# Optimization experiments

Measured on AMD Instinct MI355X. Metric: run time of the kernel, lower is better.

Reference implementation:

```python
import jax, jax.numpy as jnp
import numpy as np

NU = 200000   # num user nodes
NI = 200000   # num item nodes
E = 500000    # edges per relation
D = 128       # in_feats
H = 128       # h_feats
NEG_SLOPE = 0.01  # F.leaky_relu default


def _sage(x_src, x_dst, src, dst, n_dst, W_self, W_neigh, b):
    # DGL SAGEConv('mean'): fc_self(x_dst) + fc_neigh(mean of in-neighbors) + bias
    msg = x_src[src]                                   # [E, d] gather
    agg = jax.ops.segment_sum(msg, dst, num_segments=n_dst)   # [n_dst, d]
    deg = jax.ops.segment_sum(jnp.ones((src.shape[0],), x_src.dtype), dst,
                              num_segments=n_dst)      # [n_dst]
    mean = agg / jnp.maximum(deg, 1.0)[:, None]        # zero in-degree -> 0
    return x_dst @ W_self + mean @ W_neigh + b


def setup_inputs() -> dict:
    key = jax.random.key(0)
    ks = jax.random.split(key, 20)
    s = 1.0 / np.sqrt(D)
    inp = {
        'x_user': jax.random.normal(ks[0], (NU, D), jnp.float32),
        'x_item': jax.random.normal(ks[1], (NI, D), jnp.float32),
        'w1_self_uc': jax.random.normal(ks[2], (D, H), jnp.float32) * s,
        'w1_neigh_uc': jax.random.normal(ks[3], (D, H), jnp.float32) * s,
        'b1_uc': jnp.zeros((H,), jnp.float32),
        'w1_self_iu': jax.random.normal(ks[4], (D, H), jnp.float32) * s,
        'w1_neigh_iu': jax.random.normal(ks[5], (D, H), jnp.float32) * s,
        'b1_iu': jnp.zeros((H,), jnp.float32),
        'w2_self_uc': jax.random.normal(ks[6], (H, H), jnp.float32) * s,
        'w2_neigh_uc': jax.random.normal(ks[7], (H, H), jnp.float32) * s,
        'b2_uc': jnp.zeros((H,), jnp.float32),
        'w2_self_iu': jax.random.normal(ks[8], (H, H), jnp.float32) * s,
        'w2_neigh_iu': jax.random.normal(ks[9], (H, H), jnp.float32) * s,
        'b2_iu': jnp.zeros((H,), jnp.float32),
        'src_uc': jax.random.randint(ks[10], (E,), 0, NU, jnp.int32),
        'dst_uc': jax.random.randint(ks[11], (E,), 0, NI, jnp.int32),
        'src_iu': jax.random.randint(ks[12], (E,), 0, NI, jnp.int32),
        'dst_iu': jax.random.randint(ks[13], (E,), 0, NU, jnp.int32),
    }
    return inp


def reference(x_user, x_item,
              w1_self_uc, w1_neigh_uc, b1_uc, w1_self_iu, w1_neigh_iu, b1_iu,
              w2_self_uc, w2_neigh_uc, b2_uc, w2_self_iu, w2_neigh_iu, b2_iu,
              src_uc, dst_uc, src_iu, dst_iu):
    # layer 1: relation 'clicks' user->item, relation 'clicked_by' item->user
    h1_item = _sage(x_user, x_item, src_uc, dst_uc, NI, w1_self_uc, w1_neigh_uc, b1_uc)
    h1_user = _sage(x_item, x_user, src_iu, dst_iu, NU, w1_self_iu, w1_neigh_iu, b1_iu)
    h1_item = jax.nn.leaky_relu(h1_item, NEG_SLOPE)
    h1_user = jax.nn.leaky_relu(h1_user, NEG_SLOPE)
    # layer 2
    h2_item = _sage(h1_user, h1_item, src_uc, dst_uc, NI, w2_self_uc, w2_neigh_uc, b2_uc)
    h2_user = _sage(h1_item, h1_user, src_iu, dst_iu, NU, w2_self_iu, w2_neigh_iu, b2_iu)
    # stack [user, item] (same shape) for a single output tensor
    return jnp.stack([h2_user, h2_item], axis=0)  # [2, 200000, 128]
```

## Files before the change

kernel.cpp:

```cpp
#include <hip/hip_runtime.h>
#include <hip/hip_bf16.h>

#define D_ 128
#define H_ 128

typedef __attribute__((ext_vector_type(8))) short s8b;
typedef __attribute__((ext_vector_type(4))) float f4;

union U4 { uint u[4]; s8b v; uint4 q; };

__global__ void deg2_kernel(const int* __restrict__ dstA, const int* __restrict__ dstB,
                            int* __restrict__ degA, int* __restrict__ degB, int E) {
    int e = blockIdx.x * blockDim.x + threadIdx.x;
    const int* dst = blockIdx.y ? dstB : dstA;
    int* deg = blockIdx.y ? degB : degA;
    if (e < E) atomicAdd(&deg[dst[e]], 1);
}

__global__ __launch_bounds__(256)
void scan1m(const int* __restrict__ degA, const int* __restrict__ degB,
            int* __restrict__ rpA, int* __restrict__ rpB,
            int* __restrict__ partA, int* __restrict__ partB, int N) {
    const int* deg = blockIdx.y ? degB : degA;
    int* rp = blockIdx.y ? rpB : rpA;
    int* partials = blockIdx.y ? partB : partA;
    int tid = threadIdx.x;
    int i = blockIdx.x * 256 + tid;
    int v = (i < N) ? deg[i] : 0;
    int lane = tid & 63, wid = tid >> 6;
    int x = v;
#pragma unroll
    for (int off = 1; off < 64; off <<= 1) {
        int y = __shfl_up(x, off, 64);
        if (lane >= off) x += y;
    }
    __shared__ int wsum[5];
    if (lane == 63) wsum[wid] = x;
    __syncthreads();
    if (tid == 0) {
        int a = wsum[0], b = wsum[1], c = wsum[2], d = wsum[3];
        wsum[0] = 0; wsum[1] = a; wsum[2] = a + b; wsum[3] = a + b + c;
        wsum[4] = a + b + c + d;
    }
    __syncthreads();
    if (i < N) rp[i] = wsum[wid] + x - v;
    if (tid == 0) partials[blockIdx.x] = wsum[4];
}

__global__ __launch_bounds__(1024)
void scan2m(int* __restrict__ partA, int* __restrict__ partB, int B) {
    int* partials = blockIdx.x ? partB : partA;
    __shared__ int buf[1024];
    int t = threadIdx.x;
    int v = (t < B) ? partials[t] : 0;
    buf[t] = v;
    __syncthreads();
    for (int off = 1; off < 1024; off <<= 1) {
        int add = (t >= off) ? buf[t - off] : 0;
        __syncthreads();
        buf[t] += add;
        __syncthreads();
    }
    if (t < B) partials[t] = buf[t] - v;
}

__global__ __launch_bounds__(256)
void scan3m(int* __restrict__ rpA, int* __restrict__ rpB,
            const int* __restrict__ partA, const int* __restrict__ partB, int N, int E) {
    int* rp = blockIdx.y ? rpB : rpA;
    const int* partials = blockIdx.y ? partB : partA;
    int i = blockIdx.x * 256 + threadIdx.x;
    if (i < N) rp[i] += partials[blockIdx.x];
    if (i == 0) rp[N] = E;
}

__global__ void fill2_csr(const int* __restrict__ srcA, const int* __restrict__ dstA,
                          const int* __restrict__ rpA, int* __restrict__ curA,
                          int* __restrict__ colA, int* __restrict__ colpA,
                          const int* __restrict__ srcB, const int* __restrict__ dstB,
                          const int* __restrict__ rpB, int* __restrict__ curB,
                          int* __restrict__ colB, int* __restrict__ colpB, int E) {
    int e = blockIdx.x * blockDim.x + threadIdx.x;
    if (e >= E) return;
    const int* src = blockIdx.y ? srcB : srcA;
    const int* dst = blockIdx.y ? dstB : dstA;
    const int* rp  = blockIdx.y ? rpB : rpA;
    int* cursor = blockIdx.y ? curB : curA;
    int* col    = blockIdx.y ? colB : colA;
    int* colp   = blockIdx.y ? colpB : colpA;
    int d = dst[e];
    int s = src[e];
    int idx = atomicAdd(&cursor[d], 1);
    col[rp[d] + idx] = s;
    if (idx < 4) colp[d * 4 + idx] = s;
}

__device__ __forceinline__ void fma4(float4& a, const float4& u, float w) {
    a.x = fmaf(u.x, w, a.x); a.y = fmaf(u.y, w, a.y);
    a.z = fmaf(u.z, w, a.z); a.w = fmaf(u.w, w, a.w);
}

__device__ __forceinline__ void gather_node(const float* __restrict__ x,
                                            const int* __restrict__ rp,
                                            const int* __restrict__ col,
                                            const int* __restrict__ colp,
                                            float* __restrict__ out,
                                            int node, int li) {
    int beg = rp[node];
    int end = rp[node + 1];
    int dg = end - beg;
    int4 c4 = *(const int4*)(colp + (size_t)node * 4);
    int s0 = dg > 0 ? c4.x : 0;
    int s1 = dg > 1 ? c4.y : 0;
    int s2 = dg > 2 ? c4.z : 0;
    int s3 = dg > 3 ? c4.w : 0;
    const float4* p0 = (const float4*)(x + (size_t)s0 * 128 + li * 8);
    const float4* p1 = (const float4*)(x + (size_t)s1 * 128 + li * 8);
    const float4* p2 = (const float4*)(x + (size_t)s2 * 128 + li * 8);
    const float4* p3 = (const float4*)(x + (size_t)s3 * 128 + li * 8);
    float4 u00 = p0[0], u01 = p0[1];
    float4 u10 = p1[0], u11 = p1[1];
    float4 u20 = p2[0], u21 = p2[1];
    float4 u30 = p3[0], u31 = p3[1];
    float w0 = dg > 0 ? 1.f : 0.f;
    float w1 = dg > 1 ? 1.f : 0.f;
    float w2 = dg > 2 ? 1.f : 0.f;
    float w3 = dg > 3 ? 1.f : 0.f;
    float4 a0 = make_float4(0.f, 0.f, 0.f, 0.f);
    float4 a1 = make_float4(0.f, 0.f, 0.f, 0.f);
    fma4(a0, u00, w0); fma4(a1, u01, w0);
    fma4(a0, u10, w1); fma4(a1, u11, w1);
    fma4(a0, u20, w2); fma4(a1, u21, w2);
    fma4(a0, u30, w3); fma4(a1, u31, w3);
    for (int e = beg + 4; e < end; ++e) {
        int s = col[e];
        const float4* p = (const float4*)(x + (size_t)s * 128 + li * 8);
        float4 v0 = p[0], v1 = p[1];
        a0.x += v0.x; a0.y += v0.y; a0.z += v0.z; a0.w += v0.w;
        a1.x += v1.x; a1.y += v1.y; a1.z += v1.z; a1.w += v1.w;
    }
    float inv = 1.0f / (float)(dg > 0 ? dg : 1);
    float4 o0 = make_float4(a0.x * inv, a0.y * inv, a0.z * inv, a0.w * inv);
    float4 o1 = make_float4(a1.x * inv, a1.y * inv, a1.z * inv, a1.w * inv);
    float4* q = (float4*)(out + (size_t)node * 128 + li * 8);
    q[0] = o0;
    q[1] = o1;
}

__global__ __launch_bounds__(256)
void gather2(const float* __restrict__ xA, const int* __restrict__ rpA,
             const int* __restrict__ colA, const int* __restrict__ colpA,
             float* __restrict__ outA, int NA,
             const float* __restrict__ xB, const int* __restrict__ rpB,
             const int* __restrict__ colB, const int* __restrict__ colpB,
             float* __restrict__ outB, int NB, int blocksA) {
    bool isA = (int)blockIdx.x < blocksA;
    int bid = isA ? blockIdx.x : blockIdx.x - blocksA;
    long long gid = (long long)bid * 256 + threadIdx.x;
    int node = (int)(gid >> 4);
    int li = (int)(gid & 15);
    if (isA) {
        if (node < NA) gather_node(xA, rpA, colA, colpA, outA, node, li);
    } else {
        if (node < NB) gather_node(xB, rpB, colB, colpB, outB, node, li);
    }
}

__global__ __launch_bounds__(256)
void prep_weights(const float* __restrict__ s0, const float* __restrict__ n0,
                  const float* __restrict__ s1, const float* __restrict__ n1,
                  const float* __restrict__ s2, const float* __restrict__ n2,
                  const float* __restrict__ s3, const float* __restrict__ n3,
                  ushort* __restrict__ WTH, ushort* __restrict__ WTL) {
    int g = blockIdx.y;
    int t = blockIdx.x * 256 + threadIdx.x;
    int c = t & 127;
    int oct = t >> 7;
    const float* self  = g == 0 ? s0 : g == 1 ? s1 : g == 2 ? s2 : s3;
    const float* neigh = g == 0 ? n0 : g == 1 ? n1 : g == 2 ? n2 : n3;
    uint hd[4], ld_[4];
#pragma unroll
    for (int p = 0; p < 4; ++p) {
        uint hpair = 0, lpair = 0;
#pragma unroll
        for (int q = 0; q < 2; ++q) {
            int kv = oct * 8 + p * 2 + q;
            const float* Wsrc = kv < 128 ? self : neigh;
            float f = Wsrc[(size_t)(kv & 127) * 128 + c];
            uint u = __float_as_uint(f);
            uint h = u >> 16;
            float r = f - __uint_as_float(u & 0xffff0000u);
            uint v = __float_as_uint(r);
            uint l = (v + 0x7fffu + ((v >> 16) & 1u)) >> 16;
            hpair |= h << (16 * q);
            lpair |= l << (16 * q);
        }
        hd[p] = hpair; ld_[p] = lpair;
    }
    size_t base = ((size_t)g * 128 + c) * 256 + oct * 8;
    *(uint4*)(WTH + base) = make_uint4(hd[0], hd[1], hd[2], hd[3]);
    *(uint4*)(WTL + base) = make_uint4(ld_[0], ld_[1], ld_[2], ld_[3]);
}

__device__ __forceinline__ void gemm_body(const float* __restrict__ A1,
                                          const float* __restrict__ A2,
                                          const ushort* __restrict__ WTh,
                                          const ushort* __restrict__ WTl,
                                          const float* __restrict__ bias,
                                          float* __restrict__ out,
                                          int N, int lrelu, int bid,
                                          s8b* ldsAh, s8b* ldsAl, s8b* ldsWh, s8b* ldsWl) {
    const int t = threadIdx.x;
    const int row0 = bid * 128;
    const int lane = t & 63, w = t >> 6;
    const int mrow0 = (w & 1) * 64, ncol0 = (w >> 1) * 64;
    const int fr = lane & 15, hi = lane >> 4;

    f4 acc[4][4];
    float bv[4];
#pragma unroll
    for (int n = 0; n < 4; ++n) bv[n] = bias[ncol0 + n * 16 + fr];
#pragma unroll
    for (int m = 0; m < 4; ++m)
#pragma unroll
        for (int n = 0; n < 4; ++n) acc[m][n] = (f4){bv[n], bv[n], bv[n], bv[n]};

    const int sr = t >> 1, half = t & 1;
    const int grow = row0 + sr;
    const int swz = (sr >> 1) & 3;

    int aslot[4], wslot[4];
#pragma unroll
    for (int m = 0; m < 4; ++m) {
        int r = mrow0 + m * 16 + fr;
        aslot[m] = r * 4 + (hi ^ ((r >> 1) & 3));
    }
#pragma unroll
    for (int n = 0; n < 4; ++n) {
        int c = ncol0 + n * 16 + fr;
        wslot[n] = c * 4 + (hi ^ ((c >> 1) & 3));
    }

    for (int ks = 0; ks < 8; ++ks) {
        const float* __restrict__ As = (ks < 4) ? A1 : A2;
        const int k0 = (ks & 3) * 32 + half * 16;
        float e[16];
        if (grow < N) {
            const float4* p = (const float4*)(As + (size_t)grow * 128 + k0);
            float4 q0 = p[0], q1 = p[1], q2 = p[2], q3 = p[3];
            e[0] = q0.x; e[1] = q0.y; e[2] = q0.z; e[3] = q0.w;
            e[4] = q1.x; e[5] = q1.y; e[6] = q1.z; e[7] = q1.w;
            e[8] = q2.x; e[9] = q2.y; e[10] = q2.z; e[11] = q2.w;
            e[12] = q3.x; e[13] = q3.y; e[14] = q3.z; e[15] = q3.w;
        } else {
#pragma unroll
            for (int i = 0; i < 16; ++i) e[i] = 0.f;
        }
        uint hd[8], ld_[8];
#pragma unroll
        for (int p = 0; p < 8; ++p) {
            uint u0 = __float_as_uint(e[2 * p]);
            uint u1 = __float_as_uint(e[2 * p + 1]);
            hd[p] = (u0 >> 16) | (u1 & 0xffff0000u);
            float r0 = e[2 * p] - __uint_as_float(u0 & 0xffff0000u);
            float r1 = e[2 * p + 1] - __uint_as_float(u1 & 0xffff0000u);
            uint v0 = __float_as_uint(r0), v1 = __float_as_uint(r1);
            uint l0 = (v0 + 0x7fffu + ((v0 >> 16) & 1u)) >> 16;
            uint l1 = (v1 + 0x7fffu + ((v1 >> 16) & 1u)) >> 16;
            ld_[p] = l0 | (l1 << 16);
        }
        {
            U4 a0; a0.u[0] = hd[0]; a0.u[1] = hd[1]; a0.u[2] = hd[2]; a0.u[3] = hd[3];
            U4 a1; a1.u[0] = hd[4]; a1.u[1] = hd[5]; a1.u[2] = hd[6]; a1.u[3] = hd[7];
            U4 b0; b0.u[0] = ld_[0]; b0.u[1] = ld_[1]; b0.u[2] = ld_[2]; b0.u[3] = ld_[3];
            U4 b1; b1.u[0] = ld_[4]; b1.u[1] = ld_[5]; b1.u[2] = ld_[6]; b1.u[3] = ld_[7];
            int h0 = half * 2, h1 = half * 2 + 1;
            ldsAh[sr * 4 + (h0 ^ swz)] = a0.v;
            ldsAh[sr * 4 + (h1 ^ swz)] = a1.v;
            ldsAl[sr * 4 + (h0 ^ swz)] = b0.v;
            ldsAl[sr * 4 + (h1 ^ swz)] = b1.v;
        }
        {
            size_t wbase = (size_t)sr * 256 + ks * 32 + half * 16;
            U4 wh0, wh1, wl0, wl1;
            wh0.q = *(const uint4*)(WTh + wbase);
            wh1.q = *(const uint4*)(WTh + wbase + 8);
            wl0.q = *(const uint4*)(WTl + wbase);
            wl1.q = *(const uint4*)(WTl + wbase + 8);
            int h0 = half * 2, h1 = half * 2 + 1;
            ldsWh[sr * 4 + (h0 ^ swz)] = wh0.v;
            ldsWh[sr * 4 + (h1 ^ swz)] = wh1.v;
            ldsWl[sr * 4 + (h0 ^ swz)] = wl0.v;
            ldsWl[sr * 4 + (h1 ^ swz)] = wl1.v;
        }
        __syncthreads();

        s8b ah[4], al[4];
#pragma unroll
        for (int m = 0; m < 4; ++m) { ah[m] = ldsAh[aslot[m]]; al[m] = ldsAl[aslot[m]]; }
#pragma unroll
        for (int n = 0; n < 4; ++n) {
            s8b wh = ldsWh[wslot[n]];
            s8b wl = ldsWl[wslot[n]];
#pragma unroll
            for (int m = 0; m < 4; ++m) {
                acc[m][n] = __builtin_amdgcn_mfma_f32_16x16x32_bf16(ah[m], wh, acc[m][n], 0, 0, 0);
                acc[m][n] = __builtin_amdgcn_mfma_f32_16x16x32_bf16(al[m], wh, acc[m][n], 0, 0, 0);
                acc[m][n] = __builtin_amdgcn_mfma_f32_16x16x32_bf16(ah[m], wl, acc[m][n], 0, 0, 0);
            }
        }
        __syncthreads();
    }

#pragma unroll
    for (int m = 0; m < 4; ++m) {
#pragma unroll
        for (int r = 0; r < 4; ++r) {
            int row = row0 + mrow0 + m * 16 + hi * 4 + r;
            if (row >= N) continue;
#pragma unroll
            for (int n = 0; n < 4; ++n) {
                float v = acc[m][n][r];
                if (lrelu) v = v > 0.f ? v : 0.01f * v;
                out[(size_t)row * 128 + ncol0 + n * 16 + fr] = v;
            }
        }
    }
}

__global__ __launch_bounds__(256)
void gemm2(const float* __restrict__ A1a, const float* __restrict__ A2a,
           const ushort* __restrict__ WTha, const ushort* __restrict__ WTla,
           const float* __restrict__ ba, float* __restrict__ outa, int Na,
           const float* __restrict__ A1b, const float* __restrict__ A2b,
           const ushort* __restrict__ WThb, const ushort* __restrict__ WTlb,
           const float* __restrict__ bb, float* __restrict__ outb, int Nb,
           int blocksA, int lrelu) {
    __shared__ s8b ldsAh[512];
    __shared__ s8b ldsAl[512];
    __shared__ s8b ldsWh[512];
    __shared__ s8b ldsWl[512];
    bool isA = (int)blockIdx.x < blocksA;
    int bid = isA ? blockIdx.x : blockIdx.x - blocksA;
    if (isA)
        gemm_body(A1a, A2a, WTha, WTla, ba, outa, Na, lrelu, bid, ldsAh, ldsAl, ldsWh, ldsWl);
    else
        gemm_body(A1b, A2b, WThb, WTlb, bb, outb, Nb, lrelu, bid, ldsAh, ldsAl, ldsWh, ldsWl);
}

extern "C" void kernel_launch(void* const* d_in, const int* in_sizes, int n_in,
                              void* d_out, int out_size, void* d_ws, size_t ws_size,
                              hipStream_t stream) {
    const float* x_user     = (const float*)d_in[0];
    const float* x_item     = (const float*)d_in[1];
    const float* w1_self_uc = (const float*)d_in[2];
    const float* w1_neigh_uc= (const float*)d_in[3];
    const float* b1_uc      = (const float*)d_in[4];
    const float* w1_self_iu = (const float*)d_in[5];
    const float* w1_neigh_iu= (const float*)d_in[6];
    const float* b1_iu      = (const float*)d_in[7];
    const float* w2_self_uc = (const float*)d_in[8];
    const float* w2_neigh_uc= (const float*)d_in[9];
    const float* b2_uc      = (const float*)d_in[10];
    const float* w2_self_iu = (const float*)d_in[11];
    const float* w2_neigh_iu= (const float*)d_in[12];
    const float* b2_iu      = (const float*)d_in[13];
    const int* src_uc = (const int*)d_in[14];
    const int* dst_uc = (const int*)d_in[15];
    const int* src_iu = (const int*)d_in[16];
    const int* dst_iu = (const int*)d_in[17];

    const int NU = in_sizes[0] / D_;
    const int NI = in_sizes[1] / D_;
    const int E  = in_sizes[14];

    float* out_user = (float*)d_out;
    float* out_item = (float*)d_out + (size_t)NU * H_;

    char* ws = (char*)d_ws;
    const size_t FEAT_BYTES = (size_t)200000 * 128 * sizeof(float);
    float* agg_i   = (float*)ws;  ws += FEAT_BYTES;
    float* agg_u   = (float*)ws;  ws += FEAT_BYTES;
    ushort* WTH    = (ushort*)ws; ws += (size_t)4 * 128 * 256 * sizeof(ushort);
    ushort* WTL    = (ushort*)ws; ws += (size_t)4 * 128 * 256 * sizeof(ushort);
    int* colp_uc   = (int*)ws;    ws += (size_t)200000 * 4 * sizeof(int);
    int* colp_iu   = (int*)ws;    ws += (size_t)200000 * 4 * sizeof(int);
    int* rp_uc     = (int*)ws;    ws += (size_t)(NI + 1) * sizeof(int);
    int* rp_iu     = (int*)ws;    ws += (size_t)(NU + 1) * sizeof(int);
    int* col_uc    = (int*)ws;    ws += (size_t)E * sizeof(int);
    int* col_iu    = (int*)ws;    ws += (size_t)E * sizeof(int);
    int* deg_uc    = (int*)ws;    ws += (size_t)200000 * sizeof(int);
    int* deg_iu    = (int*)ws;    ws += (size_t)200000 * sizeof(int);
    int* cur_uc    = (int*)ws;    ws += (size_t)200000 * sizeof(int);
    int* cur_iu    = (int*)ws;    ws += (size_t)200000 * sizeof(int);
    int* partA     = (int*)ws;    ws += (size_t)1024 * sizeof(int);
    int* partB     = (int*)ws;    ws += (size_t)1024 * sizeof(int);

    const int TPB = 256;
    const int eBlocks  = (E + TPB - 1) / TPB;
    const int sBlocks  = (200000 + 255) / 256;
    const int gBlocksI = (int)(((long long)NI * 16 + TPB - 1) / TPB);
    const int gBlocksU = (int)(((long long)NU * 16 + TPB - 1) / TPB);
    const int mBlocksI = (NI + 127) / 128;
    const int mBlocksU = (NU + 127) / 128;
    const size_t WSTRIDE = (size_t)128 * 256;

    hipMemsetAsync(deg_uc, 0, (size_t)4 * 200000 * sizeof(int), stream);

    prep_weights<<<dim3(16, 4), 256, 0, stream>>>(
        w1_self_uc, w1_neigh_uc, w1_self_iu, w1_neigh_iu,
        w2_self_uc, w2_neigh_uc, w2_self_iu, w2_neigh_iu, WTH, WTL);

    deg2_kernel<<<dim3(eBlocks, 2), TPB, 0, stream>>>(dst_uc, dst_iu, deg_uc, deg_iu, E);
    scan1m<<<dim3(sBlocks, 2), 256, 0, stream>>>(deg_uc, deg_iu, rp_uc, rp_iu, partA, partB, 200000);
    scan2m<<<2, 1024, 0, stream>>>(partA, partB, sBlocks);
    scan3m<<<dim3(sBlocks, 2), 256, 0, stream>>>(rp_uc, rp_iu, partA, partB, 200000, E);
    fill2_csr<<<dim3(eBlocks, 2), TPB, 0, stream>>>(src_uc, dst_uc, rp_uc, cur_uc, col_uc, colp_uc,
                                                    src_iu, dst_iu, rp_iu, cur_iu, col_iu, colp_iu, E);

    gather2<<<gBlocksI + gBlocksU, TPB, 0, stream>>>(
        x_user, rp_uc, col_uc, colp_uc, agg_i, NI,
        x_item, rp_iu, col_iu, colp_iu, agg_u, NU, gBlocksI);
    gemm2<<<mBlocksI + mBlocksU, TPB, 0, stream>>>(
        x_item, agg_i, WTH + 0 * WSTRIDE, WTL + 0 * WSTRIDE, b1_uc, out_item, NI,
        x_user, agg_u, WTH + 1 * WSTRIDE, WTL + 1 * WSTRIDE, b1_iu, out_user, NU,
        mBlocksI, 1);

    gather2<<<gBlocksI + gBlocksU, TPB, 0, stream>>>(
        out_user, rp_uc, col_uc, colp_uc, agg_i, NI,
        out_item, rp_iu, col_iu, colp_iu, agg_u, NU, gBlocksI);
    gemm2<<<mBlocksI + mBlocksU, TPB, 0, stream>>>(
        out_item, agg_i, WTH + 2 * WSTRIDE, WTL + 2 * WSTRIDE, b2_uc, out_item, NI,
        out_user, agg_u, WTH + 3 * WSTRIDE, WTL + 3 * WSTRIDE, b2_iu, out_user, NU,
        mBlocksI, 0);
}
```

Baseline: 645.2 us.

## Store intermediates as pre-split bf16 hi/lo and double-buffer GEMM via direct LDS loads

Result: slower. 770.4 us (+19.4%).

```diff
diff --git a/kernel.cpp b/kernel.cpp
--- a/kernel.cpp
+++ b/kernel.cpp
@@ -2,12 +2,28 @@
 #include <hip/hip_bf16.h>
 
 #define D_ 128
-#define H_ 128
 
 typedef __attribute__((ext_vector_type(8))) short s8b;
 typedef __attribute__((ext_vector_type(4))) float f4;
 
 union U4 { uint u[4]; s8b v; uint4 q; };
+
+__device__ __forceinline__ void gl16(const void* g, void* lds) {
+    __builtin_amdgcn_global_load_lds(
+        (const __attribute__((address_space(1))) void*)g,
+        (__attribute__((address_space(3))) void*)lds, 16, 0, 0);
+}
+
+__device__ __forceinline__ void split2(float f0, float f1, uint& hp, uint& lp) {
+    uint u0 = __float_as_uint(f0), u1 = __float_as_uint(f1);
+    hp = (u0 >> 16) | (u1 & 0xffff0000u);
+    float r0 = f0 - __uint_as_float(u0 & 0xffff0000u);
+    float r1 = f1 - __uint_as_float(u1 & 0xffff0000u);
+    uint v0 = __float_as_uint(r0), v1 = __float_as_uint(r1);
+    uint l0 = (v0 + 0x7fffu + ((v0 >> 16) & 1u)) >> 16;
+    uint l1 = (v1 + 0x7fffu + ((v1 >> 16) & 1u)) >> 16;
+    lp = l0 | (l1 << 16);
+}
 
 __global__ void deg2_kernel(const int* __restrict__ dstA, const int* __restrict__ dstB,
                             int* __restrict__ degA, int* __restrict__ degB, int E) {
@@ -95,75 +111,97 @@
     if (idx < 4) colp[d * 4 + idx] = s;
 }
 
-__device__ __forceinline__ void fma4(float4& a, const float4& u, float w) {
-    a.x = fmaf(u.x, w, a.x); a.y = fmaf(u.y, w, a.y);
-    a.z = fmaf(u.z, w, a.z); a.w = fmaf(u.w, w, a.w);
-}
-
-__device__ __forceinline__ void gather_node(const float* __restrict__ x,
-                                            const int* __restrict__ rp,
-                                            const int* __restrict__ col,
-                                            const int* __restrict__ colp,
-                                            float* __restrict__ out,
-                                            int node, int li) {
-    int beg = rp[node];
-    int end = rp[node + 1];
+__device__ __forceinline__ void acc8hl(float* a, uint4 h4, uint4 l4, float wgt) {
+    const ushort* hu = (const ushort*)&h4;
+    const ushort* lu = (const ushort*)&l4;
+#pragma unroll
+    for (int j = 0; j < 8; ++j) {
+        float v = __uint_as_float((uint)hu[j] << 16) + __uint_as_float((uint)lu[j] << 16);
+        a[j] = fmaf(v, wgt, a[j]);
+    }
+}
+__device__ __forceinline__ void acc8f(float* a, float4 u0, float4 u1, float wgt) {
+    a[0] = fmaf(u0.x, wgt, a[0]); a[1] = fmaf(u0.y, wgt, a[1]);
+    a[2] = fmaf(u0.z, wgt, a[2]); a[3] = fmaf(u0.w, wgt, a[3]);
+    a[4] = fmaf(u1.x, wgt, a[4]); a[5] = fmaf(u1.y, wgt, a[5]);
+    a[6] = fmaf(u1.z, wgt, a[6]); a[7] = fmaf(u1.w, wgt, a[7]);
+}
+
+template<int INHL>
+__device__ __forceinline__ void gather_node(const char* x, const int* rp,
+        const int* col, const int* colp, ushort* out, int node, int li) {
+    int beg = rp[node], end = rp[node + 1];
     int dg = end - beg;
     int4 c4 = *(const int4*)(colp + (size_t)node * 4);
     int s0 = dg > 0 ? c4.x : 0;
     int s1 = dg > 1 ? c4.y : 0;
     int s2 = dg > 2 ? c4.z : 0;
     int s3 = dg > 3 ? c4.w : 0;
-    const float4* p0 = (const float4*)(x + (size_t)s0 * 128 + li * 8);
-    const float4* p1 = (const float4*)(x + (size_t)s1 * 128 + li * 8);
-    const float4* p2 = (const float4*)(x + (size_t)s2 * 128 + li * 8);
-    const float4* p3 = (const float4*)(x + (size_t)s3 * 128 + li * 8);
-    float4 u00 = p0[0], u01 = p0[1];
-    float4 u10 = p1[0], u11 = p1[1];
-    float4 u20 = p2[0], u21 = p2[1];
-    float4 u30 = p3[0], u31 = p3[1];
     float w0 = dg > 0 ? 1.f : 0.f;
     float w1 = dg > 1 ? 1.f : 0.f;
     float w2 = dg > 2 ? 1.f : 0.f;
     float w3 = dg > 3 ? 1.f : 0.f;
-    float4 a0 = make_float4(0.f, 0.f, 0.f, 0.f);
-    float4 a1 = make_float4(0.f, 0.f, 0.f, 0.f);
-    fma4(a0, u00, w0); fma4(a1, u01, w0);
-    fma4(a0, u10, w1); fma4(a1, u11, w1);
-    fma4(a0, u20, w2); fma4(a1, u21, w2);
-    fma4(a0, u30, w3); fma4(a1, u31, w3);
+    float a[8];
+#pragma unroll
+    for (int j = 0; j < 8; ++j) a[j] = 0.f;
+
+    if (INHL) {
+        const char* p0 = x + (size_t)s0 * 512 + li * 16;
+        const char* p1 = x + (size_t)s1 * 512 + li * 16;
+        const char* p2 = x + (size_t)s2 * 512 + li * 16;
+        const char* p3 = x + (size_t)s3 * 512 + li * 16;
+        uint4 H0 = *(const uint4*)p0, L0 = *(const uint4*)(p0 + 256);
+        uint4 H1 = *(const uint4*)p1, L1 = *(const uint4*)(p1 + 256);
+        uint4 H2 = *(const uint4*)p2, L2 = *(const uint4*)(p2 + 256);
+        uint4 H3 = *(const uint4*)p3, L3 = *(const uint4*)(p3 + 256);
+        acc8hl(a, H0, L0, w0); acc8hl(a, H1, L1, w1);
+        acc8hl(a, H2, L2, w2); acc8hl(a, H3, L3, w3);
+    } else {
+        const char* p0 = x + (size_t)s0 * 512 + li * 32;
+        const char* p1 = x + (size_t)s1 * 512 + li * 32;
+        const char* p2 = x + (size_t)s2 * 512 + li * 32;
+        const char* p3 = x + (size_t)s3 * 512 + li * 32;
+        float4 A0 = *(const float4*)p0, B0 = *(const float4*)(p0 + 16);
+        float4 A1 = *(const float4*)p1, B1 = *(const float4*)(p1 + 16);
+        float4 A2 = *(const float4*)p2, B2 = *(const float4*)(p2 + 16);
+        float4 A3 = *(const float4*)p3, B3 = *(const float4*)(p3 + 16);
+        acc8f(a, A0, B0, w0); acc8f(a, A1, B1, w1);
+        acc8f(a, A2, B2, w2); acc8f(a, A3, B3, w3);
+    }
     for (int e = beg + 4; e < end; ++e) {
         int s = col[e];
-        const float4* p = (const float4*)(x + (size_t)s * 128 + li * 8);
-        float4 v0 = p[0], v1 = p[1];
-        a0.x += v0.x; a0.y += v0.y; a0.z += v0.z; a0.w += v0.w;
-        a1.x += v1.x; a1.y += v1.y; a1.z += v1.z; a1.w += v1.w;
-    }
-    float inv = 1.0f / (float)(dg > 0 ? dg : 1);
-    float4 o0 = make_float4(a0.x * inv, a0.y * inv, a0.z * inv, a0.w * inv);
-    float4 o1 = make_float4(a1.x * inv, a1.y * inv, a1.z * inv, a1.w * inv);
-    float4* q = (float4*)(out + (size_t)node * 128 + li * 8);
-    q[0] = o0;
-    q[1] = o1;
-}
-
+        if (INHL) {
+            const char* p = x + (size_t)s * 512 + li * 16;
+            acc8hl(a, *(const uint4*)p, *(const uint4*)(p + 256), 1.f);
+        } else {
+            const char* p = x + (size_t)s * 512 + li * 32;
+            acc8f(a, *(const float4*)p, *(const float4*)(p + 16), 1.f);
+        }
+    }
+    float inv = 1.f / (float)(dg > 0 ? dg : 1);
+    uint h0, h1, h2, h3, l0, l1, l2, l3;
+    split2(a[0] * inv, a[1] * inv, h0, l0);
+    split2(a[2] * inv, a[3] * inv, h1, l1);
+    split2(a[4] * inv, a[5] * inv, h2, l2);
+    split2(a[6] * inv, a[7] * inv, h3, l3);
+    char* ob = (char*)out + (size_t)node * 512;
+    *(uint4*)(ob + li * 16) = make_uint4(h0, h1, h2, h3);
+    *(uint4*)(ob + 256 + li * 16) = make_uint4(l0, l1, l2, l3);
+}
+
+template<int INHL>
 __global__ __launch_bounds__(256)
-void gather2(const float* __restrict__ xA, const int* __restrict__ rpA,
-             const int* __restrict__ colA, const int* __restrict__ colpA,
-             float* __restrict__ outA, int NA,
-             const float* __restrict__ xB, const int* __restrict__ rpB,
-             const int* __restrict__ colB, const int* __restrict__ colpB,
-             float* __restrict__ outB, int NB, int blocksA) {
+void gather2k(const void* xA, const int* rpA, const int* colA, const int* colpA,
+              ushort* outA, int NA,
+              const void* xB, const int* rpB, const int* colB, const int* colpB,
+              ushort* outB, int NB, int blocksA) {
     bool isA = (int)blockIdx.x < blocksA;
     int bid = isA ? blockIdx.x : blockIdx.x - blocksA;
     long long gid = (long long)bid * 256 + threadIdx.x;
     int node = (int)(gid >> 4);
     int li = (int)(gid & 15);
-    if (isA) {
-        if (node < NA) gather_node(xA, rpA, colA, colpA, outA, node, li);
-    } else {
-        if (node < NB) gather_node(xB, rpB, colB, colpB, outB, node, li);
-    }
+    if (isA) { if (node < NA) gather_node<INHL>((const char*)xA, rpA, colA, colpA, outA, node, li); }
+    else     { if (node < NB) gather_node<INHL>((const char*)xB, rpB, colB, colpB, outB, node, li); }
 }
 
 __global__ __launch_bounds__(256)
@@ -202,150 +240,172 @@
     *(uint4*)(WTL + base) = make_uint4(ld_[0], ld_[1], ld_[2], ld_[3]);
 }
 
-__device__ __forceinline__ void gemm_body(const float* __restrict__ A1,
-                                          const float* __restrict__ A2,
-                                          const ushort* __restrict__ WTh,
-                                          const ushort* __restrict__ WTl,
-                                          const float* __restrict__ bias,
-                                          float* __restrict__ out,
-                                          int N, int lrelu, int bid,
-                                          s8b* ldsAh, s8b* ldsAl, s8b* ldsWh, s8b* ldsWl) {
+template<int A1FP32, int SPLIT, int LRELU>
+__device__ __forceinline__ void gemm_body(const void* A1, const ushort* A2,
+        const ushort* WTh, const ushort* WTl, const float* bias, void* outp,
+        int N, int bid, char* smem) {
     const int t = threadIdx.x;
+    const int w = t >> 6, lane = t & 63;
+    const int fr = lane & 15, hi = lane >> 4;
+    const int mrow0 = (w & 1) * 64, ncol0 = (w >> 1) * 64;
     const int row0 = bid * 128;
-    const int lane = t & 63, w = t >> 6;
-    const int mrow0 = (w & 1) * 64, ncol0 = (w >> 1) * 64;
-    const int fr = lane & 15, hi = lane >> 4;
 
     f4 acc[4][4];
-    float bv[4];
-#pragma unroll
-    for (int n = 0; n < 4; ++n) bv[n] = bias[ncol0 + n * 16 + fr];
+    {
+        float bv[4];
+#pragma unroll
+        for (int n = 0; n < 4; ++n) bv[n] = bias[ncol0 + n * 16 + fr];
+#pragma unroll
+        for (int m = 0; m < 4; ++m)
+#pragma unroll
+            for (int n = 0; n < 4; ++n) acc[m][n] = (f4){bv[n], bv[n], bv[n], bv[n]};
+    }
+
+    auto stage = [&](int buf, int kss) {
+        char* lb = smem + buf * 32768;
+        if (A1FP32 && kss < 4) {
+            const char* src = (const char*)A1;
+#pragma unroll
+            for (int q2 = 0; q2 < 2; ++q2) {
+                int q = w * 2 + q2;
+#pragma unroll
+                for (int half = 0; half < 2; ++half) {
+                    int gr = row0 + half * 64 + lane;
+                    gr = gr < N ? gr : N - 1;
+                    gl16(src + (size_t)gr * 512 + kss * 128 + q * 16,
+                         lb + q * 2048 + half * 1024);
+                }
+            }
+        } else {
+            const char* src = (const char*)(kss < 4 ? A1 : (const void*)A2);
+            int kk = kss & 3;
+#pragma unroll
+            for (int part = 0; part < 2; ++part) {
+#pragma unroll
+                for (int half = 0; half < 2; ++half) {
+                    int gr = row0 + half * 64 + lane;
+                    gr = gr < N ? gr : N - 1;
+                    gl16(src + (size_t)gr * 512 + kk * 64 + w * 16 + part * 256,
+                         lb + part * 8192 + w * 2048 + half * 1024);
+                }
+            }
+        }
+#pragma unroll
+        for (int part = 0; part < 2; ++part) {
+            const char* srcw = (const char*)(part ? WTl : WTh);
+#pragma unroll
+            for (int half = 0; half < 2; ++half) {
+                int col = half * 64 + lane;
+                gl16(srcw + (size_t)col * 512 + kss * 64 + w * 16,
+                     lb + 16384 + part * 8192 + w * 2048 + half * 1024);
+            }
+        }
+    };
+
+    stage(0, 0);
+    __syncthreads();
+    int buf = 0;
+    for (int ks = 0; ks < 8; ++ks) {
+        if (ks < 7) stage(buf ^ 1, ks + 1);
+        char* lb = smem + buf * 32768;
+        s8b ah[4], al[4], wh[4], wl[4];
+        if (A1FP32 && ks < 4) {
+#pragma unroll
+            for (int m = 0; m < 4; ++m) {
+                int r = mrow0 + m * 16 + fr;
+                f4 x0 = *(const f4*)(lb + (hi * 2) * 2048 + r * 16);
+                f4 x1 = *(const f4*)(lb + (hi * 2 + 1) * 2048 + r * 16);
+                U4 H, L;
+                split2(x0[0], x0[1], H.u[0], L.u[0]);
+                split2(x0[2], x0[3], H.u[1], L.u[1]);
+                split2(x1[0], x1[1], H.u[2], L.u[2]);
+                split2(x1[2], x1[3], H.u[3], L.u[3]);
+                ah[m] = H.v; al[m] = L.v;
+            }
+        } else {
+#pragma unroll
+            for (int m = 0; m < 4; ++m) {
+                int r = mrow0 + m * 16 + fr;
+                ah[m] = *(const s8b*)(lb + hi * 2048 + r * 16);
+                al[m] = *(const s8b*)(lb + 8192 + hi * 2048 + r * 16);
+            }
+        }
+#pragma unroll
+        for (int n = 0; n < 4; ++n) {
+            int c = ncol0 + n * 16 + fr;
+            wh[n] = *(const s8b*)(lb + 16384 + hi * 2048 + c * 16);
+            wl[n] = *(const s8b*)(lb + 24576 + hi * 2048 + c * 16);
+        }
+#pragma unroll
+        for (int n = 0; n < 4; ++n)
+#pragma unroll
+            for (int m = 0; m < 4; ++m) {
+                acc[m][n] = __builtin_amdgcn_mfma_f32_16x16x32_bf16(ah[m], wh[n], acc[m][n], 0, 0, 0);
+                acc[m][n] = __builtin_amdgcn_mfma_f32_16x16x32_bf16(al[m], wh[n], acc[m][n], 0, 0, 0);
+                acc[m][n] = __builtin_amdgcn_mfma_f32_16x16x32_bf16(ah[m], wl[n], acc[m][n], 0, 0, 0);
+            }
+        __syncthreads();
+        buf ^= 1;
+    }
+
+    float* T = (float*)smem;
 #pragma unroll
     for (int m = 0; m < 4; ++m)
 #pragma unroll
-        for (int n = 0; n < 4; ++n) acc[m][n] = (f4){bv[n], bv[n], bv[n], bv[n]};
-
-    const int sr = t >> 1, half = t & 1;
-    const int grow = row0 + sr;
-    const int swz = (sr >> 1) & 3;
-
-    int aslot[4], wslot[4];
-#pragma unroll
-    for (int m = 0; m < 4; ++m) {
-        int r = mrow0 + m * 16 + fr;
-        aslot[m] = r * 4 + (hi ^ ((r >> 1) & 3));
-    }
-#pragma unroll
-    for (int n = 0; n < 4; ++n) {
-        int c = ncol0 + n * 16 + fr;
-        wslot[n] = c * 4 + (hi ^ ((c >> 1) & 3));
-    }
-
-    for (int ks = 0; ks < 8; ++ks) {
-        const float* __restrict__ As = (ks < 4) ? A1 : A2;
-        const int k0 = (ks & 3) * 32 + half * 16;
-        float e[16];
-        if (grow < N) {
-            const float4* p = (const float4*)(As + (size_t)grow * 128 + k0);
-            float4 q0 = p[0], q1 = p[1], q2 = p[2], q3 = p[3];
-            e[0] = q0.x; e[1] = q0.y; e[2] = q0.z; e[3] = q0.w;
-            e[4] = q1.x; e[5] = q1.y; e[6] = q1.z; e[7] = q1.w;
-            e[8] = q2.x; e[9] = q2.y; e[10] = q2.z; e[11] = q2.w;
-            e[12] = q3.x; e[13] = q3.y; e[14] = q3.z; e[15] = q3.w;
-        } else {
-#pragma unroll
-            for (int i = 0; i < 16; ++i) e[i] = 0.f;
-        }
-        uint hd[8], ld_[8];
-#pragma unroll
-        for (int p = 0; p < 8; ++p) {
-            uint u0 = __float_as_uint(e[2 * p]);
-            uint u1 = __float_as_uint(e[2 * p + 1]);
-            hd[p] = (u0 >> 16) | (u1 & 0xffff0000u);
-            float r0 = e[2 * p] - __uint_as_float(u0 & 0xffff0000u);
-            float r1 = e[2 * p + 1] - __uint_as_float(u1 & 0xffff0000u);
-            uint v0 = __float_as_uint(r0), v1 = __float_as_uint(r1);
-            uint l0 = (v0 + 0x7fffu + ((v0 >> 16) & 1u)) >> 16;
-            uint l1 = (v1 + 0x7fffu + ((v1 >> 16) & 1u)) >> 16;
-            ld_[p] = l0 | (l1 << 16);
-        }
-        {
-            U4 a0; a0.u[0] = hd[0]; a0.u[1] = hd[1]; a0.u[2] = hd[2]; a0.u[3] = hd[3];
-            U4 a1; a1.u[0] = hd[4]; a1.u[1] = hd[5]; a1.u[2] = hd[6]; a1.u[3] = hd[7];
-            U4 b0; b0.u[0] = ld_[0]; b0.u[1] = ld_[1]; b0.u[2] = ld_[2]; b0.u[3] = ld_[3];
-            U4 b1; b1.u[0] = ld_[4]; b1.u[1] = ld_[5]; b1.u[2] = ld_[6]; b1.u[3] = ld_[7];
-            int h0 = half * 2, h1 = half * 2 + 1;
-            ldsAh[sr * 4 + (h0 ^ swz)] = a0.v;
-            ldsAh[sr * 4 + (h1 ^ swz)] = a1.v;
-            ldsAl[sr * 4 + (h0 ^ swz)] = b0.v;
-            ldsAl[sr * 4 + (h1 ^ swz)] = b1.v;
-        }
-        {
-            size_t wbase = (size_t)sr * 256 + ks * 32 + half * 16;
-            U4 wh0, wh1, wl0, wl1;
-            wh0.q = *(const uint4*)(WTh + wbase);
-            wh1.q = *(const uint4*)(WTh + wbase + 8);
-            wl0.q = *(const uint4*)(WTl + wbase);
-            wl1.q = *(const uint4*)(WTl + wbase + 8);
-            int h0 = half * 2, h1 = half * 2 + 1;
-            ldsWh[sr * 4 + (h0 ^ swz)] = wh0.v;
-            ldsWh[sr * 4 + (h1 ^ swz)] = wh1.v;
-            ldsWl[sr * 4 + (h0 ^ swz)] = wl0.v;
-            ldsWl[sr * 4 + (h1 ^ swz)] = wl1.v;
-        }
-        __syncthreads();
-
-        s8b ah[4], al[4];
-#pragma unroll
-        for (int m = 0; m < 4; ++m) { ah[m] = ldsAh[aslot[m]]; al[m] = ldsAl[aslot[m]]; }
-#pragma unroll
-        for (int n = 0; n < 4; ++n) {
-            s8b wh = ldsWh[wslot[n]];
-            s8b wl = ldsWl[wslot[n]];
-#pragma unroll
-            for (int m = 0; m < 4; ++m) {
-                acc[m][n] = __builtin_amdgcn_mfma_f32_16x16x32_bf16(ah[m], wh, acc[m][n], 0, 0, 0);
-                acc[m][n] = __builtin_amdgcn_mfma_f32_16x16x32_bf16(al[m], wh, acc[m][n], 0, 0, 0);
-                acc[m][n] = __builtin_amdgcn_mfma_f32_16x16x32_bf16(ah[m], wl, acc[m][n], 0, 0, 0);
-            }
-        }
-        __syncthreads();
-    }
-
-#pragma unroll
-    for (int m = 0; m < 4; ++m) {
-#pragma unroll
-        for (int r = 0; r < 4; ++r) {
-            int row = row0 + mrow0 + m * 16 + hi * 4 + r;
-            if (row >= N) continue;
-#pragma unroll
-            for (int n = 0; n < 4; ++n) {
-                float v = acc[m][n][r];
-                if (lrelu) v = v > 0.f ? v : 0.01f * v;
-                out[(size_t)row * 128 + ncol0 + n * 16 + fr] = v;
-            }
-        }
-    }
-}
-
+        for (int n = 0; n < 4; ++n)
+#pragma unroll
+            for (int r = 0; r < 4; ++r)
+                T[(mrow0 + m * 16 + hi * 4 + r) * 132 + ncol0 + n * 16 + fr] = acc[m][n][r];
+    __syncthreads();
+    {
+        int row = t >> 1, ch = t & 1;
+        int gr = row0 + row;
+        if (gr < N) {
+#pragma unroll
+            for (int i = 0; i < 8; ++i) {
+                const float* p = T + row * 132 + ch * 64 + i * 8;
+                f4 x0 = *(const f4*)p;
+                f4 x1 = *(const f4*)(p + 4);
+                float e0 = x0[0], e1 = x0[1], e2 = x0[2], e3 = x0[3];
+                float e4 = x1[0], e5 = x1[1], e6 = x1[2], e7 = x1[3];
+                if (LRELU) {
+                    e0 = e0 > 0.f ? e0 : 0.01f * e0;
+                    e1 = e1 > 0.f ? e1 : 0.01f * e1;
+                    e2 = e2 > 0.f ? e2 : 0.01f * e2;
+                    e3 = e3 > 0.f ? e3 : 0.01f * e3;
+                    e4 = e4 > 0.f ? e4 : 0.01f * e4;
+                    e5 = e5 > 0.f ? e5 : 0.01f * e5;
+                    e6 = e6 > 0.f ? e6 : 0.01f * e6;
+                    e7 = e7 > 0.f ? e7 : 0.01f * e7;
+                }
+                if (SPLIT) {
+                    uint h0, h1, h2, h3, l0, l1, l2, l3;
+                    split2(e0, e1, h0, l0); split2(e2, e3, h1, l1);
+                    split2(e4, e5, h2, l2); split2(e6, e7, h3, l3);
+                    char* ob = (char*)outp + (size_t)gr * 512;
+                    *(uint4*)(ob + ch * 128 + i * 16) = make_uint4(h0, h1, h2, h3);
+                    *(uint4*)(ob + 256 + ch * 128 + i * 16) = make_uint4(l0, l1, l2, l3);
+                } else {
+                    float* ob = (float*)outp + (size_t)gr * 128;
+                    *(float4*)(ob + ch * 64 + i * 8) = make_float4(e0, e1, e2, e3);
+                    *(float4*)(ob + ch * 64 + i * 8 + 4) = make_float4(e4, e5, e6, e7);
+                }
+            }
+        }
+    }
+}
+
+template<int A1FP32, int SPLIT, int LRELU>
 __global__ __launch_bounds__(256)
-void gemm2(const float* __restrict__ A1a, const float* __restrict__ A2a,
-           const ushort* __restrict__ WTha, const ushort* __restrict__ WTla,
-           const float* __restrict__ ba, float* __restrict__ outa, int Na,
-           const float* __restrict__ A1b, const float* __restrict__ A2b,
-           const ushort* __restrict__ WThb, const ushort* __restrict__ WTlb,
-           const float* __restrict__ bb, float* __restrict__ outb, int Nb,
-           int blocksA, int lrelu) {
-    __shared__ s8b ldsAh[512];
-    __shared__ s8b ldsAl[512];
-    __shared__ s8b ldsWh[512];
-    __shared__ s8b ldsWl[512];
+void gemm2k(const void* A1a, const ushort* A2a, const ushort* WTha, const ushort* WTla,
+            const float* ba, void* outa, int Na,
+            const void* A1b, const ushort* A2b, const ushort* WThb, const ushort* WTlb,
+            const float* bb, void* outb, int Nb, int blocksA) {
+    __shared__ __align__(16) char smem[67584];
     bool isA = (int)blockIdx.x < blocksA;
     int bid = isA ? blockIdx.x : blockIdx.x - blocksA;
-    if (isA)
-        gemm_body(A1a, A2a, WTha, WTla, ba, outa, Na, lrelu, bid, ldsAh, ldsAl, ldsWh, ldsWl);
-    else
-        gemm_body(A1b, A2b, WThb, WTlb, bb, outb, Nb, lrelu, bid, ldsAh, ldsAl, ldsWh, ldsWl);
+    if (isA) gemm_body<A1FP32, SPLIT, LRELU>(A1a, A2a, WTha, WTla, ba, outa, Na, bid, smem);
+    else     gemm_body<A1FP32, SPLIT, LRELU>(A1b, A2b, WThb, WTlb, bb, outb, Nb, bid, smem);
 }
 
 extern "C" void kernel_launch(void* const* d_in, const int* in_sizes, int n_in,
@@ -374,13 +434,15 @@
     const int NI = in_sizes[1] / D_;
     const int E  = in_sizes[14];
 
-    float* out_user = (float*)d_out;
-    float* out_item = (float*)d_out + (size_t)NU * H_;
+    char* hl_user = (char*)d_out;
+    char* hl_item = (char*)d_out + (size_t)NU * 512;
+    float* f_user = (float*)d_out;
+    float* f_item = (float*)d_out + (size_t)NU * 128;
 
     char* ws = (char*)d_ws;
-    const size_t FEAT_BYTES = (size_t)200000 * 128 * sizeof(float);
-    float* agg_i   = (float*)ws;  ws += FEAT_BYTES;
-    float* agg_u   = (float*)ws;  ws += FEAT_BYTES;
+    const size_t FEAT_BYTES = (size_t)200000 * 512;
+    ushort* agg_i  = (ushort*)ws; ws += FEAT_BYTES;
+    ushort* agg_u  = (ushort*)ws; ws += FEAT_BYTES;
     ushort* WTH    = (ushort*)ws; ws += (size_t)4 * 128 * 256 * sizeof(ushort);
     ushort* WTL    = (ushort*)ws; ws += (size_t)4 * 128 * 256 * sizeof(ushort);
     int* colp_uc   = (int*)ws;    ws += (size_t)200000 * 4 * sizeof(int);
@@ -418,19 +480,19 @@
     fill2_csr<<<dim3(eBlocks, 2), TPB, 0, stream>>>(src_uc, dst_uc, rp_uc, cur_uc, col_uc, colp_uc,
                                                     src_iu, dst_iu, rp_iu, cur_iu, col_iu, colp_iu, E);
 
-    gather2<<<gBlocksI + gBlocksU, TPB, 0, stream>>>(
+    gather2k<0><<<gBlocksI + gBlocksU, TPB, 0, stream>>>(
         x_user, rp_uc, col_uc, colp_uc, agg_i, NI,
         x_item, rp_iu, col_iu, colp_iu, agg_u, NU, gBlocksI);
-    gemm2<<<mBlocksI + mBlocksU, TPB, 0, stream>>>(
-        x_item, agg_i, WTH + 0 * WSTRIDE, WTL + 0 * WSTRIDE, b1_uc, out_item, NI,
-        x_user, agg_u, WTH + 1 * WSTRIDE, WTL + 1 * WSTRIDE, b1_iu, out_user, NU,
-        mBlocksI, 1);
-
-    gather2<<<gBlocksI + gBlocksU, TPB, 0, stream>>>(
-        out_user, rp_uc, col_uc, colp_uc, agg_i, NI,
-        out_item, rp_iu, col_iu, colp_iu, agg_u, NU, gBlocksI);
-    gemm2<<<mBlocksI + mBlocksU, TPB, 0, stream>>>(
-        out_item, agg_i, WTH + 2 * WSTRIDE, WTL + 2 * WSTRIDE, b2_uc, out_item, NI,
-        out_user, agg_u, WTH + 3 * WSTRIDE, WTL + 3 * WSTRIDE, b2_iu, out_user, NU,
-        mBlocksI, 0);
-}
+    gemm2k<1, 1, 1><<<mBlocksI + mBlocksU, TPB, 0, stream>>>(
+        x_item, agg_i, WTH + 0 * WSTRIDE, WTL + 0 * WSTRIDE, b1_uc, hl_item, NI,
+        x_user, agg_u, WTH + 1 * WSTRIDE, WTL + 1 * WSTRIDE, b1_iu, hl_user, NU,
+        mBlocksI);
+
+    gather2k<1><<<gBlocksI + gBlocksU, TPB, 0, stream>>>(
+        hl_user, rp_uc, col_uc, colp_uc, agg_i, NI,
+        hl_item, rp_iu, col_iu, colp_iu, agg_u, NU, gBlocksI);
+    gemm2k<0, 0, 0><<<mBlocksI + mBlocksU, TPB, 0, stream>>>(
+        hl_item, agg_i, WTH + 2 * WSTRIDE, WTL + 2 * WSTRIDE, b2_uc, f_item, NI,
+        hl_user, agg_u, WTH + 3 * WSTRIDE, WTL + 3 * WSTRIDE, b2_iu, f_user, NU,
+        mBlocksI);
+}
```
